# Performance work log

Hardware: AMD Instinct MI355X
Metric: run time of the kernel (lower is better)

Reference implementation:

```python
import jax, jax.numpy as jnp
import numpy as np

B, S, E, H = 4, 2048, 1024, 16
D = E // H  # head_dim = 64


def setup_inputs() -> dict:
    key = jax.random.key(0)
    ks = jax.random.split(key, 10)
    scale = 1.0 / np.sqrt(E)
    return {
        "decoder_sequence": jax.random.normal(ks[0], (B, S, E), dtype=jnp.float32),
        # stacked per-head projection weights (math-equivalent to per-head nn.Linear)
        "Wq": jax.random.normal(ks[1], (H, E, D), dtype=jnp.float32) * scale,
        "bq": jnp.zeros((H, D), dtype=jnp.float32),
        "Wk": jax.random.normal(ks[2], (H, E, D), dtype=jnp.float32) * scale,
        "bk": jnp.zeros((H, D), dtype=jnp.float32),
        "Wv": jax.random.normal(ks[3], (H, E, D), dtype=jnp.float32) * scale,
        "bv": jnp.zeros((H, D), dtype=jnp.float32),
        "Wo": jax.random.normal(ks[4], (E, E), dtype=jnp.float32) * scale,
        "bo": jnp.zeros((E,), dtype=jnp.float32),
    }


def reference(decoder_sequence, Wq, bq, Wk, bk, Wv, bv, Wo, bo):
    x = decoder_sequence  # [B,S,E]
    # per-head Q/K/V projections, batched over the head axis
    Q = jnp.einsum('bse,hed->bhsd', x, Wq) + bq[:, None, :]
    K = jnp.einsum('bse,hed->bhsd', x, Wk) + bk[:, None, :]
    V = jnp.einsum('bse,hed->bhsd', x, Wv) + bv[:, None, :]
    # scaled scores with causal mask (upper triangle -> -inf)
    A = jnp.einsum('bhid,bhjd->bhij', Q, K) / jnp.sqrt(jnp.float32(D))
    causal = jnp.tril(jnp.ones((S, S), dtype=bool))  # True where allowed
    A = jnp.where(causal, A, -jnp.inf)
    A = jax.nn.softmax(A, axis=-1)
    Hout = jnp.einsum('bhij,bhjd->bhid', A, V)  # [B,H,S,D]
    # concat heads: [B,S,H*D]
    concat = jnp.transpose(Hout, (0, 2, 1, 3)).reshape(B, S, H * D)
    return concat @ Wo.T + bo
```

## Files before the change

kernel.cpp:

```cpp
#include <hip/hip_runtime.h>
#include <stdint.h>
#include <stddef.h>

typedef __bf16 bf16;
typedef __bf16 bf16x8 __attribute__((ext_vector_type(8)));
typedef __bf16 bf16x4 __attribute__((ext_vector_type(4)));
typedef float  f32x4  __attribute__((ext_vector_type(4)));
typedef float  f32x16 __attribute__((ext_vector_type(16)));
typedef unsigned short ush;
typedef ush ush8 __attribute__((ext_vector_type(8)));
typedef unsigned int uint;

#define B_  4
#define S_  2048
#define E_  1024
#define H_  16
#define D_  64
#define M_  (B_*S_)
#define K_  E_
#define QSCALE 0.18033688011112042f

__device__ __forceinline__ void gload_lds16(const void* g, void* l) {
  __builtin_amdgcn_global_load_lds((const __attribute__((address_space(1))) void*)g,
                                   (__attribute__((address_space(3))) void*)l, 16, 0, 0);
}
__device__ __forceinline__ f32x4 mfma16(bf16x8 a, bf16x8 b, f32x4 c) {
  return __builtin_amdgcn_mfma_f32_16x16x32_bf16(a, b, c, 0, 0, 0);
}
__device__ __forceinline__ f32x16 mfma32(bf16x8 a, bf16x8 b, f32x16 c) {
  return __builtin_amdgcn_mfma_f32_32x32x16_bf16(a, b, c, 0, 0, 0);
}
__device__ __forceinline__ int swz4(int row, int ch) { return ch ^ ((row >> 1) & 3); }
__device__ __forceinline__ uint cvtpk(float lo, float hi) {
  uint r;
  asm("v_cvt_pk_bf16_f32 %0, %1, %2" : "=v"(r) : "v"(lo), "v"(hi));
  return r;
}

__global__ void cast_f32_bf16(const float* __restrict__ src, bf16* __restrict__ dst, int n4) {
  int idx = blockIdx.x * blockDim.x + threadIdx.x;
  int stride = gridDim.x * blockDim.x;
  for (int i = idx; i < n4; i += stride) {
    float4 v = ((const float4*)src)[i];
    union { bf16 b[4]; ushort4 u; } cv;
    cv.b[0] = (bf16)v.x; cv.b[1] = (bf16)v.y; cv.b[2] = (bf16)v.z; cv.b[3] = (bf16)v.w;
    ((ushort4*)dst)[i] = cv.u;
  }
}

__global__ void pack_w_t(const float* __restrict__ Wq, const float* __restrict__ Wk,
                         const float* __restrict__ Wv, bf16* __restrict__ Wp) {
  __shared__ float t[64][65];
  const int tid = threadIdx.x;
  const int wh = blockIdx.y;
  const int which = wh >> 4, h = wh & 15;
  const int e0 = blockIdx.x << 6;
  const float* src = (which == 0) ? Wq : (which == 1 ? Wk : Wv);
  src += (size_t)h * (E_ * D_);
  #pragma unroll
  for (int i = 0; i < 4; ++i) {
    int fi = tid + 256 * i;
    int e = fi >> 4, c = fi & 15;
    float4 v = *(const float4*)(src + (size_t)(e0 + e) * D_ + c * 4);
    t[c * 4 + 0][e] = v.x; t[c * 4 + 1][e] = v.y;
    t[c * 4 + 2][e] = v.z; t[c * 4 + 3][e] = v.w;
  }
  __syncthreads();
  #pragma unroll
  for (int i = 0; i < 2; ++i) {
    int cid = tid + 256 * i;
    int d = cid >> 3, cc = cid & 7;
    ush8 o;
    #pragma unroll
    for (int j = 0; j < 8; ++j) {
      union { bf16 b; ush u; } cv; cv.b = (bf16)t[d][cc * 8 + j]; o[j] = cv.u;
    }
    *(ush8*)(Wp + ((size_t)which * 1024 + h * 64 + d) * K_ + e0 + cc * 8) = o;
  }
}

template <int MODE>
__launch_bounds__(256, 3)
__global__ void gemm_kernel(const bf16* __restrict__ A, const bf16* __restrict__ Bm,
                            int Ntot,
                            const float* __restrict__ bias0, const float* __restrict__ bias1,
                            const float* __restrict__ bias2,
                            bf16* __restrict__ Qo, bf16* __restrict__ Ko, bf16* __restrict__ Vto,
                            float* __restrict__ Fo) {
  __shared__ __align__(16) bf16 lds_a[2][128 * 32];
  __shared__ __align__(16) bf16 lds_b[2][128 * 32];
  const int tid = threadIdx.x;
  const int lane = tid & 63;
  const int w = tid >> 6;
  const int wr = w >> 1, wc = w & 1;
  const int nblk = Ntot >> 7;
  const int qch = gridDim.x >> 3;
  const int swz = (blockIdx.x & 7) * qch + (blockIdx.x >> 3);
  const int mt = swz / nblk, nt = swz % nblk;
  const int m0 = mt << 7, n0 = nt << 7;

  f32x4 acc[4][4] = {};

  auto stage = [&](int buf, int kt) {
    #pragma unroll
    for (int i = 0; i < 2; ++i) {
      int cb = (w * 2 + i) * 64;
      int cid = cb + lane;
      int row = cid >> 2, cir = cid & 3;
      int lch = swz4(row, cir);
      const bf16* ga = A  + (size_t)(m0 + row) * K_ + kt * 32 + lch * 8;
      const bf16* gb = Bm + (size_t)(n0 + row) * K_ + kt * 32 + lch * 8;
      gload_lds16(ga, &lds_a[buf][cb * 8]);
      gload_lds16(gb, &lds_b[buf][cb * 8]);
    }
  };

  const int NT = K_ / 32;
  stage(0, 0);
  for (int kt = 0; kt < NT; ++kt) {
    if (kt + 1 < NT) stage((kt + 1) & 1, kt + 1);
    __syncthreads();
    const bf16x8* pa = (const bf16x8*)&lds_a[kt & 1][0];
    const bf16x8* pb = (const bf16x8*)&lds_b[kt & 1][0];
    bf16x8 af[4], bfr[4];
    #pragma unroll
    for (int mb = 0; mb < 4; ++mb) {
      int row = wr * 64 + mb * 16 + (lane & 15);
      af[mb] = pa[row * 4 + swz4(row, lane >> 4)];
    }
    #pragma unroll
    for (int nb = 0; nb < 4; ++nb) {
      int row = wc * 64 + nb * 16 + (lane & 15);
      bfr[nb] = pb[row * 4 + swz4(row, lane >> 4)];
    }
    #pragma unroll
    for (int mb = 0; mb < 4; ++mb)
      #pragma unroll
      for (int nb = 0; nb < 4; ++nb)
        acc[mb][nb] = mfma16(af[mb], bfr[nb], acc[mb][nb]);
    __syncthreads();
  }

  #pragma unroll
  for (int mb = 0; mb < 4; ++mb) {
    #pragma unroll
    for (int nb = 0; nb < 4; ++nb) {
      const int ni  = n0 + wc * 64 + nb * 16 + (lane & 15);
      const int mi0 = m0 + wr * 64 + mb * 16 + (lane >> 4) * 4;
      if (MODE == 0) {
        const int which = ni >> 10;
        const int col = ni & 1023;
        const float* bp = (which == 0) ? bias0 : (which == 1 ? bias1 : bias2);
        const float bv = bp[col];
        const int hh = col >> 6, d = col & 63;
        const int b = mi0 >> 11, s0r = mi0 & 2047;
        if (which == 2) {
          bf16x4 st;
          #pragma unroll
          for (int r = 0; r < 4; ++r) st[r] = (bf16)(acc[mb][nb][r] + bv);
          *(bf16x4*)(Vto + ((size_t)((b * H_ + hh) * D_ + d)) * S_ + s0r) = st;
        } else {
          bf16* dst = (which == 0) ? Qo : Ko;
          const float sc = (which == 0) ? QSCALE : 1.f;
          #pragma unroll
          for (int r = 0; r < 4; ++r)
            dst[(((size_t)(b * H_ + hh)) * S_ + (s0r + r)) * D_ + d] =
                (bf16)((acc[mb][nb][r] + bv) * sc);
        }
      } else {
        #pragma unroll
        for (int r = 0; r < 4; ++r)
          Fo[(size_t)(mi0 + r) * E_ + ni] = acc[mb][nb][r] + bias0[ni];
      }
    }
  }
}

struct QTile {
  bf16x8 qf[4];
  f32x16 oacc[2];
  float m, l;
};

__device__ __forceinline__ void init_q(QTile& S, const bf16* qrow, int hi) {
  #pragma unroll
  for (int kc = 0; kc < 4; ++kc)
    S.qf[kc] = *(const bf16x8*)(qrow + (2 * kc + hi) * 8);
  #pragma unroll
  for (int r = 0; r < 16; ++r) { S.oacc[0][r] = 0.f; S.oacc[1][r] = 0.f; }
  S.m = -1e30f; S.l = 0.f;
}

__device__ __forceinline__ void tile_step(QTile& S, const bf16* klds, const bf16* vlds,
                                          int sub, int kv0, int qb_, int qg_, int hi, int ln) {
  if (kv0 > qb_ + 31) return;
  const bf16* kbase = klds + sub * (64 * 64);
  f32x16 s0 = {}, s1 = {};
  const int lxor = (ln & 7) ^ ((ln >> 3) & 3);
  #pragma unroll
  for (int kc = 0; kc < 4; ++kc) {
    int ch = (2 * kc + hi) ^ lxor;
    bf16x8 k0 = *(const bf16x8*)&kbase[ln * 64 + ch * 8];
    bf16x8 k1 = *(const bf16x8*)&kbase[(32 + ln) * 64 + ch * 8];
    s0 = mfma32(k0, S.qf[kc], s0);
    s1 = mfma32(k1, S.qf[kc], s1);
  }
  if (kv0 + 63 > qb_) {
    #pragma unroll
    for (int r = 0; r < 16; ++r) {
      int crow = (r & 3) + 8 * (r >> 2) + 4 * hi;
      if (kv0 + crow > qg_)      s0[r] = -1e30f;
      if (kv0 + 32 + crow > qg_) s1[r] = -1e30f;
    }
  }
  float tm[16];
  #pragma unroll
  for (int r = 0; r < 16; ++r) tm[r] = fmaxf(s0[r], s1[r]);
  #pragma unroll
  for (int st = 8; st >= 1; st >>= 1)
    #pragma unroll
    for (int r = 0; r < st; ++r) tm[r] = fmaxf(tm[r], tm[r + st]);
  float mt_ = fmaxf(tm[0], __shfl_xor(tm[0], 32, 64));
  bool resc = mt_ > S.m + 8.f;
  float mold = S.m;
  float mnew = resc ? mt_ : S.m;
  S.m = mnew;
  #pragma unroll
  for (int r = 0; r < 16; ++r) { s0[r] = exp2f(s0[r] - mnew); s1[r] = exp2f(s1[r] - mnew); }
  if (__any(resc)) {
    float alpha = resc ? exp2f(mold - mnew) : 1.f;
    S.l *= alpha;
    #pragma unroll
    for (int r = 0; r < 16; ++r) { S.oacc[0][r] *= alpha; S.oacc[1][r] *= alpha; }
  }
  bf16x8 pf[4];
  #pragma unroll
  for (int mtl = 0; mtl < 2; ++mtl) {
    #pragma unroll
    for (int c = 0; c < 2; ++c) {
      const f32x16& p = mtl ? s1 : s0;
      uint wa = cvtpk(p[8 * c + 0], p[8 * c + 1]);
      uint wb = cvtpk(p[8 * c + 2], p[8 * c + 3]);
      uint wcx = cvtpk(p[8 * c + 4], p[8 * c + 5]);
      uint wd = cvtpk(p[8 * c + 6], p[8 * c + 7]);
      asm("v_permlane32_swap_b32 %0, %1" : "+v"(wa), "+v"(wcx));
      asm("v_permlane32_swap_b32 %0, %1" : "+v"(wb), "+v"(wd));
      union { uint u[4]; bf16x8 v; } cvt;
      cvt.u[0] = wa; cvt.u[1] = wb; cvt.u[2] = wcx; cvt.u[3] = wd;
      pf[mtl * 2 + c] = cvt.v;
    }
  }
  const bf16 one_ = (bf16)1.f;
  const bf16x8 vones = {one_, one_, one_, one_, one_, one_, one_, one_};
  f32x16 lt = {};
  #pragma unroll
  for (int ks = 0; ks < 4; ++ks) lt = mfma32(vones, pf[ks], lt);
  #pragma unroll
  for (int dm = 0; dm < 2; ++dm) {
    #pragma unroll
    for (int ks = 0; ks < 4; ++ks) {
      int row = dm * 32 + ln;
      int cfull = sub * 8 + 2 * ks + hi;
      int ch = cfull ^ (ln & 15);
      bf16x8 vf = *(const bf16x8*)&vlds[row * 128 + ch * 8];
      S.oacc[dm] = mfma32(vf, pf[ks], S.oacc[dm]);
    }
  }
  S.l += lt[0];
}

__device__ __forceinline__ void store_o(const QTile& S, bf16* orow, int hi) {
  float rinv = 1.f / S.l;
  #pragma unroll
  for (int dm = 0; dm < 2; ++dm) {
    #pragma unroll
    for (int g = 0; g < 4; ++g) {
      bf16x4 st;
      #pragma unroll
      for (int i = 0; i < 4; ++i) st[i] = (bf16)(S.oacc[dm][4 * g + i] * rinv);
      *(bf16x4*)(orow + dm * 32 + g * 8 + hi * 4) = st;
    }
  }
}

__launch_bounds__(256, 2)
__global__ void attn_kernel(const bf16* __restrict__ Q, const bf16* __restrict__ K,
                            const bf16* __restrict__ Vt, bf16* __restrict__ Cc) {
  __shared__ __align__(16) bf16 k_lds[2][128 * 64];
  __shared__ __align__(16) bf16 v_lds[2][64 * 128];
  const int tid = threadIdx.x, lane = tid & 63, w = tid >> 6;
  const int hi = lane >> 5, ln = lane & 31;
  const int bid = blockIdx.x;
  const int bh = bid & 63;
  const int x = bid >> 6;
  const int jta = x, jtb = 15 - x;
  const bf16* Kb = K  + (size_t)bh * (S_ * D_);
  const bf16* Vb = Vt + (size_t)bh * (D_ * S_);
  const int b = bh >> 4, hh = bh & 15;

  auto stage2 = [&](int buf, int ph) {
    const int kv0 = ph << 7;
    #pragma unroll
    for (int i = 0; i < 4; ++i) {
      int cb = (w * 4 + i) * 64;
      int cid = cb + lane;
      int row = cid >> 3, cir = cid & 7;
      int lch = cir ^ (row & 7) ^ ((row >> 3) & 3);
      gload_lds16(Kb + (size_t)(kv0 + row) * D_ + lch * 8, &k_lds[buf][cb * 8]);
      int rowv = cid >> 4, cirv = cid & 15;
      int lchv = cirv ^ (rowv & 15);
      gload_lds16(Vb + (size_t)rowv * S_ + kv0 + lchv * 8, &v_lds[buf][cb * 8]);
    }
  };

  {
    const int qb_ = jta * 128 + w * 32, qg_ = qb_ + ln;
    QTile SA;
    init_q(SA, Q + ((size_t)bh * S_ + qg_) * D_, hi);
    const int nph = x + 1;
    stage2(0, 0);
    __syncthreads();
    for (int ph = 0; ph < nph; ++ph) {
      int cur = ph & 1;
      if (ph + 1 < nph) stage2(cur ^ 1, ph + 1);
      tile_step(SA, k_lds[cur], v_lds[cur], 0, ph * 128,      qb_, qg_, hi, ln);
      tile_step(SA, k_lds[cur], v_lds[cur], 1, ph * 128 + 64, qb_, qg_, hi, ln);
      __syncthreads();
    }
    store_o(SA, Cc + ((size_t)(b * S_ + qg_)) * E_ + hh * D_, hi);
  }
  {
    const int qb_ = jtb * 128 + w * 32, qg_ = qb_ + ln;
    QTile SB;
    init_q(SB, Q + ((size_t)bh * S_ + qg_) * D_, hi);
    const int nph = 16 - x;
    stage2(0, 0);
    __syncthreads();
    for (int ph = 0; ph < nph; ++ph) {
      int cur = ph & 1;
      if (ph + 1 < nph) stage2(cur ^ 1, ph + 1);
      tile_step(SB, k_lds[cur], v_lds[cur], 0, ph * 128,      qb_, qg_, hi, ln);
      tile_step(SB, k_lds[cur], v_lds[cur], 1, ph * 128 + 64, qb_, qg_, hi, ln);
      __syncthreads();
    }
    store_o(SB, Cc + ((size_t)(b * S_ + qg_)) * E_ + hh * D_, hi);
  }
}

extern "C" void kernel_launch(void* const* d_in, const int* in_sizes, int n_in,
                              void* d_out, int out_size, void* d_ws, size_t ws_size,
                              hipStream_t stream) {
  const float* x  = (const float*)d_in[0];
  const float* Wq = (const float*)d_in[1];
  const float* bq = (const float*)d_in[2];
  const float* Wk = (const float*)d_in[3];
  const float* bk = (const float*)d_in[4];
  const float* Wv = (const float*)d_in[5];
  const float* bv = (const float*)d_in[6];
  const float* Wo = (const float*)d_in[7];
  const float* bo = (const float*)d_in[8];
  float* out = (float*)d_out;

  uint8_t* ws = (uint8_t*)d_ws;
  bf16* Xbf   = (bf16*)(ws + 0);
  bf16* Wpack = (bf16*)(ws + 16777216);
  bf16* Wot   = (bf16*)(ws + 23068672);
  bf16* Qb    = (bf16*)(ws + 25165824);
  bf16* Kb    = (bf16*)(ws + 41943040);
  bf16* Vtb   = (bf16*)(ws + 75497472);
  bf16* Cc    = Xbf;

  cast_f32_bf16<<<2048, 256, 0, stream>>>(x,  Xbf, (M_ * K_) / 4);
  cast_f32_bf16<<<1024, 256, 0, stream>>>(Wo, Wot, (E_ * E_) / 4);
  pack_w_t<<<dim3(16, 48), 256, 0, stream>>>(Wq, Wk, Wv, Wpack);

  gemm_kernel<0><<<dim3(64 * 24), 256, 0, stream>>>(Xbf, Wpack, 3072, bq, bk, bv,
                                                    Qb, Kb, Vtb, nullptr);

  attn_kernel<<<dim3(512), 256, 0, stream>>>(Qb, Kb, Vtb, Cc);

  gemm_kernel<1><<<dim3(64 * 8), 256, 0, stream>>>(Cc, Wot, 1024, bo, nullptr, nullptr,
                                                   nullptr, nullptr, nullptr, out);
}
```

Measured before the change: 189.6 us.

## Process both paired query tiles in one fused KV pass with MFMA priority hints

The attention kernel previously handled the two causally paired query tiles (x and 15-x) in two sequential passes, each streaming K/V from global memory into LDS. It now keeps both tiles' state live and runs a single loop over the longer tile's KV range, so every staged K/V block feeds both tiles and the shorter tile's loads are no longer repeated. It also wraps the MFMA sections with s_setprio to favour matrix issue across waves. The cost is doubled accumulator and Q-fragment register state per thread, which may raise register pressure and hurt occupancy under launch_bounds(256,2).

```diff
diff --git a/kernel.cpp b/kernel.cpp
--- a/kernel.cpp
+++ b/kernel.cpp
@@ -197,6 +197,7 @@
   const bf16* kbase = klds + sub * (64 * 64);
   f32x16 s0 = {}, s1 = {};
   const int lxor = (ln & 7) ^ ((ln >> 3) & 3);
+  __builtin_amdgcn_s_setprio(1);
   #pragma unroll
   for (int kc = 0; kc < 4; ++kc) {
     int ch = (2 * kc + hi) ^ lxor;
@@ -205,6 +206,7 @@
     s0 = mfma32(k0, S.qf[kc], s0);
     s1 = mfma32(k1, S.qf[kc], s1);
   }
+  __builtin_amdgcn_s_setprio(0);
   if (kv0 + 63 > qb_) {
     #pragma unroll
     for (int r = 0; r < 16; ++r) {
@@ -253,6 +255,7 @@
   const bf16 one_ = (bf16)1.f;
   const bf16x8 vones = {one_, one_, one_, one_, one_, one_, one_, one_};
   f32x16 lt = {};
+  __builtin_amdgcn_s_setprio(1);
   #pragma unroll
   for (int ks = 0; ks < 4; ++ks) lt = mfma32(vones, pf[ks], lt);
   #pragma unroll
@@ -266,6 +269,7 @@
       S.oacc[dm] = mfma32(vf, pf[ks], S.oacc[dm]);
     }
   }
+  __builtin_amdgcn_s_setprio(0);
   S.l += lt[0];
 }
 
@@ -293,10 +297,17 @@
   const int bid = blockIdx.x;
   const int bh = bid & 63;
   const int x = bid >> 6;
-  const int jta = x, jtb = 15 - x;
   const bf16* Kb = K  + (size_t)bh * (S_ * D_);
   const bf16* Vb = Vt + (size_t)bh * (D_ * S_);
   const int b = bh >> 4, hh = bh & 15;
+
+  const int qbA = x * 128 + w * 32,        qgA = qbA + ln;
+  const int qbB = (15 - x) * 128 + w * 32, qgB = qbB + ln;
+  const int nphA = x + 1, nphB = 16 - x;
+
+  QTile SA, SB;
+  init_q(SA, Q + ((size_t)bh * S_ + qgA) * D_, hi);
+  init_q(SB, Q + ((size_t)bh * S_ + qgB) * D_, hi);
 
   auto stage2 = [&](int buf, int ph) {
     const int kv0 = ph << 7;
@@ -313,38 +324,21 @@
     }
   };
 
-  {
-    const int qb_ = jta * 128 + w * 32, qg_ = qb_ + ln;
-    QTile SA;
-    init_q(SA, Q + ((size_t)bh * S_ + qg_) * D_, hi);
-    const int nph = x + 1;
-    stage2(0, 0);
+  stage2(0, 0);
+  __syncthreads();
+  for (int ph = 0; ph < nphB; ++ph) {
+    const int cur = ph & 1;
+    if (ph + 1 < nphB) stage2(cur ^ 1, ph + 1);
+    const int kv0 = ph << 7;
+    if (ph < nphA) tile_step(SA, k_lds[cur], v_lds[cur], 0, kv0,      qbA, qgA, hi, ln);
+    tile_step(SB, k_lds[cur], v_lds[cur], 0, kv0,      qbB, qgB, hi, ln);
+    if (ph < nphA) tile_step(SA, k_lds[cur], v_lds[cur], 1, kv0 + 64, qbA, qgA, hi, ln);
+    tile_step(SB, k_lds[cur], v_lds[cur], 1, kv0 + 64, qbB, qgB, hi, ln);
     __syncthreads();
-    for (int ph = 0; ph < nph; ++ph) {
-      int cur = ph & 1;
-      if (ph + 1 < nph) stage2(cur ^ 1, ph + 1);
-      tile_step(SA, k_lds[cur], v_lds[cur], 0, ph * 128,      qb_, qg_, hi, ln);
-      tile_step(SA, k_lds[cur], v_lds[cur], 1, ph * 128 + 64, qb_, qg_, hi, ln);
-      __syncthreads();
-    }
-    store_o(SA, Cc + ((size_t)(b * S_ + qg_)) * E_ + hh * D_, hi);
-  }
-  {
-    const int qb_ = jtb * 128 + w * 32, qg_ = qb_ + ln;
-    QTile SB;
-    init_q(SB, Q + ((size_t)bh * S_ + qg_) * D_, hi);
-    const int nph = 16 - x;
-    stage2(0, 0);
-    __syncthreads();
-    for (int ph = 0; ph < nph; ++ph) {
-      int cur = ph & 1;
-      if (ph + 1 < nph) stage2(cur ^ 1, ph + 1);
-      tile_step(SB, k_lds[cur], v_lds[cur], 0, ph * 128,      qb_, qg_, hi, ln);
-      tile_step(SB, k_lds[cur], v_lds[cur], 1, ph * 128 + 64, qb_, qg_, hi, ln);
-      __syncthreads();
-    }
-    store_o(SB, Cc + ((size_t)(b * S_ + qg_)) * E_ + hh * D_, hi);
-  }
+  }
+
+  store_o(SA, Cc + ((size_t)(b * S_ + qgA)) * E_ + hh * D_, hi);
+  store_o(SB, Cc + ((size_t)(b * S_ + qgB)) * E_ + hh * D_, hi);
 }
 
 extern "C" void kernel_launch(void* const* d_in, const int* in_sizes, int n_in,
```

Result: no change. 188.7 us (-0.5%).
